# Kernel tuning notes

Hardware: AMD Instinct MI355X
Metric: run time of the kernel (lower is better)

Reference implementation:

```python
import math
import jax, jax.numpy as jnp
import numpy as np

N_NODES = 10000
N_EDGES = 160000
F_IN = 256
HID = 500
N_OUT = 100


def setup_inputs() -> dict:
    key = jax.random.key(0)
    ks = jax.random.split(key, 20)
    inp = {}
    inp['x'] = jax.random.normal(ks[0], (N_NODES, F_IN), jnp.float32)
    inp['edge_src'] = jax.random.randint(ks[1], (N_EDGES,), 0, N_NODES, jnp.int32)
    inp['edge_dst'] = jax.random.randint(ks[2], (N_EDGES,), 0, N_NODES, jnp.int32)
    inp['edge_weight'] = jax.random.uniform(ks[3], (N_EDGES,), jnp.float32)
    s1 = 1.0 / math.sqrt(F_IN)
    s2 = 1.0 / math.sqrt(HID)
    inp['W1_rel'] = jax.random.uniform(ks[4], (HID, F_IN), jnp.float32, -s1, s1)
    inp['b1'] = jax.random.uniform(ks[5], (HID,), jnp.float32, -s1, s1)
    inp['W1_root'] = jax.random.uniform(ks[6], (HID, F_IN), jnp.float32, -s1, s1)
    inp['p1_w'] = jax.random.uniform(ks[7], (HID,), jnp.float32, -s2, s2)
    inp['W2_rel'] = jax.random.uniform(ks[8], (HID, HID), jnp.float32, -s2, s2)
    inp['b2'] = jax.random.uniform(ks[9], (HID,), jnp.float32, -s2, s2)
    inp['W2_root'] = jax.random.uniform(ks[10], (HID, HID), jnp.float32, -s2, s2)
    inp['p2_w'] = jax.random.uniform(ks[11], (HID,), jnp.float32, -s2, s2)
    s3 = 1.0 / math.sqrt(1000)
    inp['lin1_W'] = jax.random.uniform(ks[12], (2000, 1000), jnp.float32, -s3, s3)
    inp['lin1_b'] = jax.random.uniform(ks[13], (2000,), jnp.float32, -s3, s3)
    s4 = 1.0 / math.sqrt(2000)
    inp['lin2_W'] = jax.random.uniform(ks[14], (4000, 2000), jnp.float32, -s4, s4)
    inp['lin2_b'] = jax.random.uniform(ks[15], (4000,), jnp.float32, -s4, s4)
    s5 = 1.0 / math.sqrt(4000)
    inp['lin3_W'] = jax.random.uniform(ks[16], (N_OUT, 4000), jnp.float32, -s5, s5)
    inp['lin3_b'] = jax.random.uniform(ks[17], (N_OUT,), jnp.float32, -s5, s5)
    return inp


def graph_conv(x, src, dst, w, W_rel, b_rel, W_root):
    # PyG GraphConv: out_i = W_rel @ sum_{j->i} w_ji * x_j + b + W_root @ x_i
    msg = x[src] * w[:, None]                              # [E, F]
    agg = jax.ops.segment_sum(msg, dst, num_segments=x.shape[0])
    return agg @ W_rel.T + b_rel + x @ W_root.T


def topk_pool(x, src, dst, w, p_w, ratio=0.5):
    # PyG TopKPooling: score = tanh(x @ p / ||p||); keep top-k; scale x by score.
    N = x.shape[0]
    k = int(math.ceil(ratio * N))
    score = jnp.tanh((x @ p_w) / jnp.linalg.norm(p_w))
    vals, perm = jax.lax.top_k(score, k)
    x_new = x[perm] * vals[:, None]
    # keep fixed-size edge list; dropped edges get weight 0 and point to node 0
    new_idx = jnp.zeros((N,), jnp.int32).at[perm].set(jnp.arange(k, dtype=jnp.int32))
    mask = jnp.zeros((N,), bool).at[perm].set(True)
    keep = mask[src] & mask[dst]
    src_new = jnp.where(keep, new_idx[src], 0)
    dst_new = jnp.where(keep, new_idx[dst], 0)
    w_new = jnp.where(keep, w, 0.0)
    return x_new, src_new, dst_new, w_new


def readout(x):
    # global max pool + global mean pool over the single graph -> [1, 2F]
    return jnp.concatenate([jnp.max(x, 0, keepdims=True), jnp.mean(x, 0, keepdims=True)], axis=1)


def reference(x, edge_src, edge_dst, edge_weight,
              W1_rel, b1, W1_root, p1_w,
              W2_rel, b2, W2_root, p2_w,
              lin1_W, lin1_b, lin2_W, lin2_b, lin3_W, lin3_b):
    h = jax.nn.relu(graph_conv(x, edge_src, edge_dst, edge_weight, W1_rel, b1, W1_root))
    h, s1, d1, w1 = topk_pool(h, edge_src, edge_dst, edge_weight, p1_w)
    x1 = readout(h)
    h = jax.nn.relu(graph_conv(h, s1, d1, w1, W2_rel, b2, W2_root))
    h, _, _, _ = topk_pool(h, s1, d1, w1, p2_w)
    x2 = readout(h)
    z = x1 + x2                                            # [1, 1000]
    z = jax.nn.relu(z @ lin1_W.T + lin1_b)
    z = jax.nn.relu(z @ lin2_W.T + lin2_b)                 # dropout is identity at eval
    return jax.nn.sigmoid(z @ lin3_W.T + lin3_b)
```

## Files before the change

kernel.cpp:

```cpp
#include <hip/hip_runtime.h>
#include <math.h>

#define NN1   10000
#define NE    160000
#define FIN   256
#define HID   500
#define K1    5000
#define NN2   5000
#define K2    2500
#define NSLAB 64
#define RORPB  79
#define RCHUNK 500

#define CSR_OFFS   0u
#define CSR_POS    10008u
#define OFF_SC1    20008u
#define OFF_SC2    30008u
#define OFF_CTR    35008u
#define ZERO_BASE  10008u
#define ZERO_LEN   25032u
#define CSR_EDGE   35040u
#define OFF_SCALE1 355040u
#define OFF_SCALE2 365040u
#define OFF_RK1    370040u
#define OFF_RK2    380040u
#define OFF_PM1    385056u
#define OFF_PS1    417056u
#define OFF_PM2    449056u
#define OFF_PS2    481056u
#define OFF_Z      513056u
#define OFF_T1     514056u
#define OFF_T2     516056u
#define OFF_INV    520056u
#define OFF_AGG    520064u
#define OFF_H      1800064u
#define OFF_XP1B   4300064u
#define OFF_XB     6175064u
#define OFF_W1RB   7455064u
#define OFF_W1TB   7519064u
#define OFF_W2RB   7583064u
#define OFF_W2TB   7708064u
#define OFF_CNT    7833088u
#define WS_FLOATS  8033120u

__device__ inline unsigned f2ord(float f) {
    unsigned u = __float_as_uint(f);
    return (u & 0x80000000u) ? ~u : (u | 0x80000000u);
}
__device__ inline unsigned long long rkey(float s, int j) {
    return ((unsigned long long)f2ord(s) << 32) | (unsigned)(0xFFFFFFFFu - (unsigned)j);
}
__device__ inline unsigned short bf16rn(float f) {
    unsigned u = __float_as_uint(f);
    u += 0x7FFFu + ((u >> 16) & 1u);
    return (unsigned short)(u >> 16);
}
__device__ inline float bf2f(unsigned short u) {
    return __uint_as_float((unsigned)u << 16);
}

typedef __attribute__((ext_vector_type(8))) short short8;
typedef __attribute__((ext_vector_type(4))) float floatx4;

__device__ inline short8 ld8g(const unsigned short* p, int gk, int K) {
    if (gk + 7 < K) return *(const short8*)p;
    unsigned short tmp[8] = {0,0,0,0,0,0,0,0};
    for (int q = 0; q < 8; ++q) if (gk + q < K) tmp[q] = p[q];
    return *(short8*)tmp;
}


__global__ __launch_bounds__(256) void k_prep(
    const float* __restrict__ x, unsigned short* __restrict__ xb,
    const float* __restrict__ w1r, unsigned short* __restrict__ w1rb,
    const float* __restrict__ w1t, unsigned short* __restrict__ w1tb,
    const float* __restrict__ w2r, unsigned short* __restrict__ w2rb,
    const float* __restrict__ w2t, unsigned short* __restrict__ w2tb,
    const float* __restrict__ p1, const float* __restrict__ p2,
    float* __restrict__ invn,
    const int* __restrict__ edst, int* __restrict__ pos) {
    __shared__ float red[256];
    int tid = threadIdx.x;
    int y = blockIdx.y;
    if (y < 5) {
        const float* s; unsigned short* d; int n4;
        switch (y) {
            case 0: s = x;   d = xb;   n4 = NN1 * FIN / 4; break;
            case 1: s = w1r; d = w1rb; n4 = HID * FIN / 4; break;
            case 2: s = w1t; d = w1tb; n4 = HID * FIN / 4; break;
            case 3: s = w2r; d = w2rb; n4 = HID * HID / 4; break;
            default: s = w2t; d = w2tb; n4 = HID * HID / 4; break;
        }
        int stride = gridDim.x * 256;
        for (int i = blockIdx.x * 256 + tid; i < n4; i += stride) {
            float4 v = *(const float4*)(s + (size_t)i * 4);
            ushort4 o;
            o.x = bf16rn(v.x); o.y = bf16rn(v.y); o.z = bf16rn(v.z); o.w = bf16rn(v.w);
            *(ushort4*)(d + (size_t)i * 4) = o;
        }
    } else if (y == 5) {
        if (blockIdx.x >= 2) return;
        const float* p = blockIdx.x ? p2 : p1;
        float s = 0.f;
        for (int i = tid; i < HID; i += 256) { float v = p[i]; s += v * v; }
        red[tid] = s; __syncthreads();
        for (int w = 128; w > 0; w >>= 1) {
            if (tid < w) red[tid] += red[tid + w];
            __syncthreads();
        }
        if (tid == 0) invn[blockIdx.x] = 1.0f / sqrtf(red[0]);
    } else {
        int stride = gridDim.x * 256;
        for (int e = blockIdx.x * 256 + tid; e < NE; e += stride)
            atomicAdd(&pos[edst[e]], 1);
    }
}

__global__ __launch_bounds__(1024) void k_scan(int* __restrict__ pos, int* __restrict__ offs) {
    __shared__ int tot[1024];
    int t = threadIdx.x;
    int base = t * 10;
    int loc[10]; int s = 0;
    #pragma unroll
    for (int q = 0; q < 10; ++q) {
        int v = (base + q < NN1) ? pos[base + q] : 0;
        loc[q] = s; s += v;
    }
    tot[t] = s; __syncthreads();
    for (int d = 1; d < 1024; d <<= 1) {
        int v = (t >= d) ? tot[t - d] : 0;
        __syncthreads();
        tot[t] += v;
        __syncthreads();
    }
    int excl = (t == 0) ? 0 : tot[t - 1];
    #pragma unroll
    for (int q = 0; q < 10; ++q)
        if (base + q < NN1) { int o = excl + loc[q]; offs[base + q] = o; pos[base + q] = o; }
    if (t == 1023) offs[NN1] = tot[1023];
}

__global__ __launch_bounds__(256) void k_fill(
    const int* __restrict__ src, const int* __restrict__ dst,
    const float* __restrict__ w, int* __restrict__ pos,
    int2* __restrict__ ce) {
    int e = blockIdx.x * 256 + threadIdx.x;
    if (e >= NE) return;
    int slot = atomicAdd(&pos[dst[e]], 1);
    ce[slot] = make_int2(src[e], __float_as_int(w[e]));
}

__global__ __launch_bounds__(256) void k_gather1(
    const unsigned short* __restrict__ xb, const int* __restrict__ offs,
    const int2* __restrict__ ce, unsigned short* __restrict__ aggb) {
    int wave = (blockIdx.x * 256 + threadIdx.x) >> 6;
    int lane = threadIdx.x & 63;
    if (wave >= NN1) return;
    int b = offs[wave], e = offs[wave + 1];
    float4 a0 = make_float4(0.f, 0.f, 0.f, 0.f);
    float4 a1 = make_float4(0.f, 0.f, 0.f, 0.f);
    int p = b;
    for (; p + 1 < e; p += 2) {
        int2 e0 = ce[p], e1 = ce[p + 1];
        float w0 = __int_as_float(e0.y), w1 = __int_as_float(e1.y);
        ushort4 u0 = *(const ushort4*)(xb + (size_t)e0.x * FIN + lane * 4);
        ushort4 u1 = *(const ushort4*)(xb + (size_t)e1.x * FIN + lane * 4);
        a0.x += bf2f(u0.x) * w0; a0.y += bf2f(u0.y) * w0;
        a0.z += bf2f(u0.z) * w0; a0.w += bf2f(u0.w) * w0;
        a1.x += bf2f(u1.x) * w1; a1.y += bf2f(u1.y) * w1;
        a1.z += bf2f(u1.z) * w1; a1.w += bf2f(u1.w) * w1;
    }
    if (p < e) {
        int2 e0 = ce[p];
        float w0 = __int_as_float(e0.y);
        ushort4 u0 = *(const ushort4*)(xb + (size_t)e0.x * FIN + lane * 4);
        a0.x += bf2f(u0.x) * w0; a0.y += bf2f(u0.y) * w0;
        a0.z += bf2f(u0.z) * w0; a0.w += bf2f(u0.w) * w0;
    }
    ushort4 o;
    o.x = bf16rn(a0.x + a1.x); o.y = bf16rn(a0.y + a1.y);
    o.z = bf16rn(a0.z + a1.z); o.w = bf16rn(a0.w + a1.w);
    *(ushort4*)(aggb + (size_t)wave * FIN + lane * 4) = o;
}

#define GBK 64
__global__ __launch_bounds__(256) void k_gemm_bf16(
    const unsigned short* __restrict__ A1, const unsigned short* __restrict__ B1,
    const unsigned short* __restrict__ A2, const unsigned short* __restrict__ B2,
    const float* __restrict__ bias, const float* __restrict__ pv,
    unsigned short* __restrict__ C, float* __restrict__ score,
    int M, int N, int Ka, int Kb, int nbyRow) {
    __shared__ unsigned short As[2][64 * 64];
    __shared__ unsigned short Bs[2][64 * 64];
    int tid = threadIdx.x;
    int b = blockIdx.x;
    int xcd = b & 7, seq = b >> 3;
    int colT = seq & 7;
    int rowT = xcd + 8 * (seq >> 3);
    if (rowT >= nbyRow) return;
    int row0 = rowT * 64, col0 = colT * 64;
    int lane = tid & 63, wid = tid >> 6;
    int waveM = wid & 1, waveN = wid >> 1;
    int quad = lane >> 4, mrow = lane & 15;
    int m7 = mrow & 7;
    floatx4 acc[2][2] = {};

    int sr = tid >> 2;
    int ca = (tid & 3) * 2;
    int s7 = sr & 7;
    int c0 = (ca ^ s7) * 8;
    int c1 = ((ca + 1) ^ s7) * 8;
    int sbase = sr * 64;

    int nka = (Ka + GBK - 1) / GBK;
    int nkb = (Kb + GBK - 1) / GBK;
    int niter = nka + nkb;

    short8 z8 = {0,0,0,0,0,0,0,0};
    short8 paA = z8, paB = z8, pbA = z8, pbB = z8;

    auto fetch = [&](int t) {
        int ph = (t >= nka);
        const unsigned short* A = ph ? A2 : A1;
        const unsigned short* B = ph ? B2 : B1;
        int K = ph ? Kb : Ka;
        int gk = (ph ? t - nka : t) * GBK + ca * 8;
        int gr = row0 + sr, gn = col0 + sr;
        paA = z8; paB = z8; pbA = z8; pbB = z8;
        if (gr < M) {
            const unsigned short* p = A + (size_t)gr * K + gk;
            paA = ld8g(p, gk, K); paB = ld8g(p + 8, gk + 8, K);
        }
        if (gn < N) {
            const unsigned short* p = B + (size_t)gn * K + gk;
            pbA = ld8g(p, gk, K); pbB = ld8g(p + 8, gk + 8, K);
        }
    };
    auto commit = [&](int buf) {
        *(short8*)&As[buf][sbase + c0] = paA;
        *(short8*)&As[buf][sbase + c1] = paB;
        *(short8*)&Bs[buf][sbase + c0] = pbA;
        *(short8*)&Bs[buf][sbase + c1] = pbB;
    };

    fetch(0);
    commit(0);
    if (niter > 1) fetch(1);
    __syncthreads();

    for (int it = 0; it < niter; ++it) {
        int cur = it & 1;
        if (it + 1 < niter) commit(cur ^ 1);
        if (it + 2 < niter) fetch(it + 2);
        #pragma unroll
        for (int half = 0; half < 2; ++half) {
            int qc = half * 4 + quad;
            int qoff = (qc ^ m7) * 8;
            short8 bfr[2];
            #pragma unroll
            for (int nt = 0; nt < 2; ++nt)
                bfr[nt] = *(short8*)&Bs[cur][(waveN * 32 + nt * 16 + mrow) * 64 + qoff];
            #pragma unroll
            for (int mt = 0; mt < 2; ++mt) {
                short8 afr = *(short8*)&As[cur][(waveM * 32 + mt * 16 + mrow) * 64 + qoff];
                #pragma unroll
                for (int nt = 0; nt < 2; ++nt)
                    acc[mt][nt] = __builtin_amdgcn_mfma_f32_16x16x32_bf16(
                        afr, bfr[nt], acc[mt][nt], 0, 0, 0);
            }
        }
        __syncthreads();
    }
    float ps[2][4] = {};
    #pragma unroll
    for (int nt = 0; nt < 2; ++nt) {
        int col = col0 + waveN * 32 + nt * 16 + mrow;
        if (col >= N) continue;
        float bv = bias[col];
        float pc = pv[col];
        #pragma unroll
        for (int mt = 0; mt < 2; ++mt) {
            int rbase = row0 + waveM * 32 + mt * 16 + quad * 4;
            #pragma unroll
            for (int r = 0; r < 4; ++r) {
                float v = fmaxf(acc[mt][nt][r] + bv, 0.f);
                int row = rbase + r;
                if (row < M) C[(size_t)row * N + col] = bf16rn(v);
                ps[mt][r] += v * pc;
            }
        }
    }
    #pragma unroll
    for (int mt = 0; mt < 2; ++mt)
        #pragma unroll
        for (int r = 0; r < 4; ++r) {
            float v = ps[mt][r];
            v += __shfl_xor(v, 1, 64); v += __shfl_xor(v, 2, 64);
            v += __shfl_xor(v, 4, 64); v += __shfl_xor(v, 8, 64);
            if (mrow == 0) {
                int row = row0 + waveM * 32 + mt * 16 + quad * 4 + r;
                if (row < M) atomicAdd(&score[row], v);
            }
        }
}

__global__ __launch_bounds__(256) void k_rank_partial(
    const float* __restrict__ score, int* __restrict__ cntp, int Nn) {
    __shared__ unsigned long long kj[RCHUNK];
    int j0 = blockIdx.y * RCHUNK;
    int jn = min(Nn - j0, RCHUNK);
    for (int t = threadIdx.x; t < jn; t += 256)
        kj[t] = rkey(score[j0 + t], j0 + t);
    __syncthreads();
    int i = blockIdx.x * 256 + threadIdx.x;
    if (i >= Nn) return;
    unsigned long long ki = rkey(score[i], i);
    int c = 0;
    #pragma unroll 4
    for (int q = 0; q < jn; ++q)
        c += (kj[q] > ki) ? 1 : 0;
    cntp[(size_t)blockIdx.y * Nn + i] = c;
}

__global__ __launch_bounds__(256) void k_gather_pool(
    const unsigned short* __restrict__ Hb, const float* __restrict__ score,
    const float* __restrict__ invn,
    const int* __restrict__ cntp, int Nn, int nchunk, int kk,
    int* __restrict__ rank_out, unsigned short* __restrict__ Xb) {
    int wave = (blockIdx.x * 256 + threadIdx.x) >> 6;
    int lane = threadIdx.x & 63;
    int nw = gridDim.x * 4;
    for (int i = wave; i < Nn; i += nw) {
        int c = (lane < nchunk) ? cntp[(size_t)lane * Nn + i] : 0;
        for (int off = 32; off > 0; off >>= 1) c += __shfl_down(c, off, 64);
        c = __shfl(c, 0, 64);
        int r = (c < kk) ? c : -1;
        if (lane == 0) rank_out[i] = r;
        if (r < 0) continue;
        float sc = tanhf(score[i] * invn[0]);
        const ushort4* src = (const ushort4*)(Hb + (size_t)i * HID);
        ushort4* dst = (ushort4*)(Xb + (size_t)r * HID);
        ushort4 u = src[lane];
        ushort4 o;
        o.x = bf16rn(bf2f(u.x) * sc); o.y = bf16rn(bf2f(u.y) * sc);
        o.z = bf16rn(bf2f(u.z) * sc); o.w = bf16rn(bf2f(u.w) * sc);
        dst[lane] = o;
        if (lane < HID / 4 - 64) {
            ushort4 u2 = src[lane + 64];
            ushort4 o2;
            o2.x = bf16rn(bf2f(u2.x) * sc); o2.y = bf16rn(bf2f(u2.y) * sc);
            o2.z = bf16rn(bf2f(u2.z) * sc); o2.w = bf16rn(bf2f(u2.w) * sc);
            dst[lane + 64] = o2;
        }
    }
}

__global__ __launch_bounds__(256) void k_rank_fin2(
    const float* __restrict__ score, const float* __restrict__ invn,
    const int* __restrict__ cntp, int Nn, int nchunk, int kk,
    int* __restrict__ rank_out, float* __restrict__ scale_out) {
    int i = blockIdx.x * 256 + threadIdx.x;
    if (i >= Nn) return;
    int t = 0;
    for (int q = 0; q < nchunk; ++q) t += cntp[(size_t)q * Nn + i];
    rank_out[i] = (t < kk) ? t : -1;
    scale_out[i] = tanhf(score[i] * invn[0]);
}

__device__ void readout_slab(const unsigned short* __restrict__ X, int rows, int rpb,
                             int slabY, int colHalf,
                             float* __restrict__ pmax, float* __restrict__ psum) {
    __shared__ float4 lmx[4][64];
    __shared__ float4 lsm[4][64];
    int lane = threadIdx.x & 63;
    int rgrp = threadIdx.x >> 6;
    int c4 = colHalf * 64 + lane;
    int r0 = slabY * rpb;
    int r1 = min(rows, r0 + rpb);
    float4 mx = make_float4(-INFINITY, -INFINITY, -INFINITY, -INFINITY);
    float4 sm = make_float4(0.f, 0.f, 0.f, 0.f);
    if (c4 < HID / 4) {
        for (int r = r0 + rgrp; r < r1; r += 4) {
            ushort4 u = *(const ushort4*)(X + (size_t)r * HID + c4 * 4);
            float vx = bf2f(u.x), vy = bf2f(u.y), vz = bf2f(u.z), vw = bf2f(u.w);
            mx.x = fmaxf(mx.x, vx); mx.y = fmaxf(mx.y, vy);
            mx.z = fmaxf(mx.z, vz); mx.w = fmaxf(mx.w, vw);
            sm.x += vx; sm.y += vy; sm.z += vz; sm.w += vw;
        }
    }
    lmx[rgrp][lane] = mx; lsm[rgrp][lane] = sm;
    __syncthreads();
    if (rgrp == 0 && c4 < HID / 4) {
        #pragma unroll
        for (int g = 1; g < 4; ++g) {
            float4 m2 = lmx[g][lane], s2 = lsm[g][lane];
            mx.x = fmaxf(mx.x, m2.x); mx.y = fmaxf(mx.y, m2.y);
            mx.z = fmaxf(mx.z, m2.z); mx.w = fmaxf(mx.w, m2.w);
            sm.x += s2.x; sm.y += s2.y; sm.z += s2.z; sm.w += s2.w;
        }
        *(float4*)(pmax + (size_t)slabY * HID + c4 * 4) = mx;
        *(float4*)(psum + (size_t)slabY * HID + c4 * 4) = sm;
    }
}

__global__ __launch_bounds__(256) void k_g2r1(
    const unsigned short* __restrict__ xp1, const int* __restrict__ offs,
    const int2* __restrict__ ce, const int* __restrict__ rank,
    unsigned short* __restrict__ aggb,
    float* __restrict__ pm1, float* __restrict__ ps1) {
    if (blockIdx.x < 2500) {
        int wave = (blockIdx.x * 256 + threadIdx.x) >> 6;
        int lane = threadIdx.x & 63;
        int rd = rank[wave];
        if (rd < 0) return;
        int b = offs[wave], e = offs[wave + 1];
        int c1 = 256 + lane * 4;
        float a0 = 0.f, a1 = 0.f, a2 = 0.f, a3 = 0.f;
        float b0 = 0.f, b1v = 0.f, b2 = 0.f, b3 = 0.f;
        int2 nxt = (b < e) ? ce[b] : make_int2(0, 0);
        for (int p = b; p < e; ++p) {
            int2 cur = nxt;
            if (p + 1 < e) nxt = ce[p + 1];
            int rs = rank[cur.x];
            if (rs < 0) continue;
            float we = __int_as_float(cur.y);
            const unsigned short* row = xp1 + (size_t)rs * HID;
            ushort4 u = *(const ushort4*)(row + lane * 4);
            a0 += bf2f(u.x) * we; a1 += bf2f(u.y) * we;
            a2 += bf2f(u.z) * we; a3 += bf2f(u.w) * we;
            if (c1 < HID) {
                ushort4 u2 = *(const ushort4*)(row + c1);
                b0 += bf2f(u2.x) * we; b1v += bf2f(u2.y) * we;
                b2 += bf2f(u2.z) * we; b3 += bf2f(u2.w) * we;
            }
        }
        unsigned short* o = aggb + (size_t)rd * HID;
        ushort4 o1; o1.x = bf16rn(a0); o1.y = bf16rn(a1); o1.z = bf16rn(a2); o1.w = bf16rn(a3);
        *(ushort4*)(o + lane * 4) = o1;
        if (c1 < HID) {
            ushort4 o2; o2.x = bf16rn(b0); o2.y = bf16rn(b1v); o2.z = bf16rn(b2); o2.w = bf16rn(b3);
            *(ushort4*)(o + c1) = o2;
        }
    } else {
        int b = blockIdx.x - 2500;
        readout_slab(xp1, K1, RORPB, b >> 1, b & 1, pm1, ps1);
    }
}

__global__ __launch_bounds__(256) void k_readout2(
    const unsigned short* __restrict__ hb, const int* __restrict__ rank2,
    const float* __restrict__ scale2,
    float* __restrict__ pm2, float* __restrict__ ps2,
    const float* __restrict__ pm1, const float* __restrict__ ps1,
    float* __restrict__ z, int* __restrict__ donectr) {
    __shared__ float4 lmx[4][64];
    __shared__ float4 lsm[4][64];
    __shared__ int flag;
    int tid = threadIdx.x;
    int lane = tid & 63;
    int rgrp = tid >> 6;
    int slabY = blockIdx.x >> 1, colHalf = blockIdx.x & 1;
    int c4 = colHalf * 64 + lane;
    int r0 = slabY * RORPB;
    int r1 = min(NN2, r0 + RORPB);
    float4 mx = make_float4(-INFINITY, -INFINITY, -INFINITY, -INFINITY);
    float4 sm = make_float4(0.f, 0.f, 0.f, 0.f);
    if (c4 < HID / 4) {
        for (int r = r0 + rgrp; r < r1; r += 4) {
            if (rank2[r] < 0) continue;
            float sc = scale2[r];
            ushort4 u = *(const ushort4*)(hb + (size_t)r * HID + c4 * 4);
            float vx = bf2f(u.x) * sc, vy = bf2f(u.y) * sc;
            float vz = bf2f(u.z) * sc, vw = bf2f(u.w) * sc;
            mx.x = fmaxf(mx.x, vx); mx.y = fmaxf(mx.y, vy);
            mx.z = fmaxf(mx.z, vz); mx.w = fmaxf(mx.w, vw);
            sm.x += vx; sm.y += vy; sm.z += vz; sm.w += vw;
        }
    }
    lmx[rgrp][lane] = mx; lsm[rgrp][lane] = sm;
    __syncthreads();
    if (rgrp == 0 && c4 < HID / 4) {
        #pragma unroll
        for (int g = 1; g < 4; ++g) {
            float4 m2 = lmx[g][lane], s2 = lsm[g][lane];
            mx.x = fmaxf(mx.x, m2.x); mx.y = fmaxf(mx.y, m2.y);
            mx.z = fmaxf(mx.z, m2.z); mx.w = fmaxf(mx.w, m2.w);
            sm.x += s2.x; sm.y += s2.y; sm.z += s2.z; sm.w += s2.w;
        }
        *(float4*)(pm2 + (size_t)slabY * HID + c4 * 4) = mx;
        *(float4*)(ps2 + (size_t)slabY * HID + c4 * 4) = sm;
    }
    if (tid == 0) {
        __threadfence();
        flag = (atomicAdd(donectr, 1) == (int)gridDim.x - 1) ? 1 : 0;
    }
    __syncthreads();
    if (!flag) return;
    __threadfence();
    for (int j = tid; j < HID; j += 256) {
        float m1 = -INFINITY, s1 = 0.f, m2v = -INFINITY, s2v = 0.f;
        for (int s = 0; s < NSLAB; ++s) {
            m1 = fmaxf(m1, pm1[(size_t)s * HID + j]); s1 += ps1[(size_t)s * HID + j];
            m2v = fmaxf(m2v, pm2[(size_t)s * HID + j]); s2v += ps2[(size_t)s * HID + j];
        }
        z[j] = m1 + m2v;
        z[HID + j] = s1 * (1.0f / (float)K1) + s2v * (1.0f / (float)K2);
    }
}

__global__ __launch_bounds__(256) void k_mv(
    const float* __restrict__ v, const float* __restrict__ W,
    const float* __restrict__ bias, float* __restrict__ y,
    int rowsN, int K, int act) {
    int wave = (blockIdx.x * 256 + threadIdx.x) >> 6;
    int lane = threadIdx.x & 63;
    if (wave >= rowsN) return;
    const float* wr = W + (size_t)wave * K;
    float s = 0.f;
    for (int c = lane * 4; c < K; c += 256) {
        float4 a = *(const float4*)(wr + c);
        float4 xv = *(const float4*)(v + c);
        s += a.x * xv.x + a.y * xv.y + a.z * xv.z + a.w * xv.w;
    }
    for (int off = 32; off > 0; off >>= 1) s += __shfl_down(s, off, 64);
    if (lane == 0) {
        float r = s + bias[wave];
        y[wave] = (act == 0) ? fmaxf(r, 0.f) : 1.f / (1.f + expf(-r));
    }
}

extern "C" void kernel_launch(void* const* d_in, const int* in_sizes, int n_in,
                              void* d_out, int out_size, void* d_ws, size_t ws_size,
                              hipStream_t stream) {
    const float* x      = (const float*)d_in[0];
    const int*   esrc   = (const int*)d_in[1];
    const int*   edst   = (const int*)d_in[2];
    const float* ew     = (const float*)d_in[3];
    const float* W1_rel = (const float*)d_in[4];
    const float* b1     = (const float*)d_in[5];
    const float* W1_root= (const float*)d_in[6];
    const float* p1     = (const float*)d_in[7];
    const float* W2_rel = (const float*)d_in[8];
    const float* b2     = (const float*)d_in[9];
    const float* W2_root= (const float*)d_in[10];
    const float* p2     = (const float*)d_in[11];
    const float* l1W    = (const float*)d_in[12];
    const float* l1b    = (const float*)d_in[13];
    const float* l2W    = (const float*)d_in[14];
    const float* l2b    = (const float*)d_in[15];
    const float* l3W    = (const float*)d_in[16];
    const float* l3b    = (const float*)d_in[17];
    float* out = (float*)d_out;
    float* ws  = (float*)d_ws;

    if (ws_size < (size_t)WS_FLOATS * sizeof(float)) return;

    int*            offs   = (int*)(ws + CSR_OFFS);
    int*            pos    = (int*)(ws + CSR_POS);
    float*          score1 = ws + OFF_SC1;
    float*          score2 = ws + OFF_SC2;
    int*            ctr    = (int*)(ws + OFF_CTR);
    int2*           ce     = (int2*)(ws + CSR_EDGE);
    float*          scale2 = ws + OFF_SCALE2;
    int*            rk1    = (int*)(ws + OFF_RK1);
    int*            rk2    = (int*)(ws + OFF_RK2);
    float*          pm1    = ws + OFF_PM1;
    float*          ps1    = ws + OFF_PS1;
    float*          pm2    = ws + OFF_PM2;
    float*          ps2    = ws + OFF_PS2;
    float*          zbuf   = ws + OFF_Z;
    float*          t1     = ws + OFF_T1;
    float*          t2     = ws + OFF_T2;
    float*          invn   = ws + OFF_INV;
    int*            cntp   = (int*)(ws + OFF_CNT);
    unsigned short* aggb   = (unsigned short*)(ws + OFF_AGG);
    unsigned short* hb     = (unsigned short*)(ws + OFF_H);
    unsigned short* xp1b   = (unsigned short*)(ws + OFF_XP1B);
    unsigned short* xb     = (unsigned short*)(ws + OFF_XB);
    unsigned short* w1rb   = (unsigned short*)(ws + OFF_W1RB);
    unsigned short* w1tb   = (unsigned short*)(ws + OFF_W1TB);
    unsigned short* w2rb   = (unsigned short*)(ws + OFF_W2RB);
    unsigned short* w2tb   = (unsigned short*)(ws + OFF_W2TB);

    hipMemsetAsync(ws + ZERO_BASE, 0, (size_t)ZERO_LEN * sizeof(float), stream);

    k_prep<<<dim3(640, 7), 256, 0, stream>>>(
        x, xb, W1_rel, w1rb, W1_root, w1tb, W2_rel, w2rb, W2_root, w2tb,
        p1, p2, invn, edst, pos);
    k_scan<<<1, 1024, 0, stream>>>(pos, offs);
    k_fill<<<(NE + 255) / 256, 256, 0, stream>>>(esrc, edst, ew, pos, ce);

    k_gather1<<<(NN1 * 64) / 256, 256, 0, stream>>>(xb, offs, ce, aggb);
    {
        int nby = (NN1 + 63) / 64;
        int nblk = 64 * ((nby + 7) / 8);
        k_gemm_bf16<<<nblk, 256, 0, stream>>>(
            aggb, w1rb, xb, w1tb, b1, p1, hb, score1, NN1, HID, FIN, FIN, nby);
    }

    k_rank_partial<<<dim3((NN1 + 255) / 256, NN1 / RCHUNK), 256, 0, stream>>>(
        score1, cntp, NN1);
    k_gather_pool<<<1250, 256, 0, stream>>>(
        hb, score1, invn + 0, cntp, NN1, NN1 / RCHUNK, K1, rk1, xp1b);

    k_g2r1<<<2500 + 2 * NSLAB, 256, 0, stream>>>(xp1b, offs, ce, rk1, aggb, pm1, ps1);
    {
        int nby = (NN2 + 63) / 64;
        int nblk = 64 * ((nby + 7) / 8);
        k_gemm_bf16<<<nblk, 256, 0, stream>>>(
            aggb, w2rb, xp1b, w2tb, b2, p2, hb, score2, NN2, HID, HID, HID, nby);
    }

    k_rank_partial<<<dim3((NN2 + 255) / 256, NN2 / RCHUNK), 256, 0, stream>>>(
        score2, cntp, NN2);
    k_rank_fin2<<<(NN2 + 255) / 256, 256, 0, stream>>>(
        score2, invn + 1, cntp, NN2, NN2 / RCHUNK, K2, rk2, scale2);

    k_readout2<<<2 * NSLAB, 256, 0, stream>>>(
        hb, rk2, scale2, pm2, ps2, pm1, ps1, zbuf, ctr + 3);

    k_mv<<<(2000 * 64) / 256, 256, 0, stream>>>(zbuf, l1W, l1b, t1, 2000, 1000, 0);
    k_mv<<<(4000 * 64) / 256, 256, 0, stream>>>(t1, l2W, l2b, t2, 4000, 2000, 0);
    k_mv<<<(100 * 64) / 256, 256, 0, stream>>>(t2, l3W, l3b, out, 100, 4000, 1);
}
```

Before: 315.9 us.

## Fuse second top-k ranking and scale into readout kernel

Removes the separate partial-rank and rank-finalize launches for the second pooling stage. Each readout block now ranks its own slab of rows by comparing score keys against all 5000 scores staged in shared memory, and computes the tanh scale locally. This saves two kernel launches and the round trip of the count buffer through global memory. In exchange, every block redoes the ranking comparisons for its rows (about 79x5000 per block) and uses about 20 KB of shared memory.

```diff
diff --git a/kernel.cpp b/kernel.cpp
--- a/kernel.cpp
+++ b/kernel.cpp
@@ -20,10 +20,7 @@
 #define ZERO_BASE  10008u
 #define ZERO_LEN   25032u
 #define CSR_EDGE   35040u
-#define OFF_SCALE1 355040u
-#define OFF_SCALE2 365040u
-#define OFF_RK1    370040u
-#define OFF_RK2    380040u
+#define OFF_RK1X   370040u
 #define OFF_PM1    385056u
 #define OFF_PS1    417056u
 #define OFF_PM2    449056u
@@ -353,18 +350,6 @@
             dst[lane + 64] = o2;
         }
     }
-}
-
-__global__ __launch_bounds__(256) void k_rank_fin2(
-    const float* __restrict__ score, const float* __restrict__ invn,
-    const int* __restrict__ cntp, int Nn, int nchunk, int kk,
-    int* __restrict__ rank_out, float* __restrict__ scale_out) {
-    int i = blockIdx.x * 256 + threadIdx.x;
-    if (i >= Nn) return;
-    int t = 0;
-    for (int q = 0; q < nchunk; ++q) t += cntp[(size_t)q * Nn + i];
-    rank_out[i] = (t < kk) ? t : -1;
-    scale_out[i] = tanhf(score[i] * invn[0]);
 }
 
 __device__ void readout_slab(const unsigned short* __restrict__ X, int rows, int rpb,
@@ -447,28 +432,55 @@
     }
 }
 
-__global__ __launch_bounds__(256) void k_readout2(
-    const unsigned short* __restrict__ hb, const int* __restrict__ rank2,
-    const float* __restrict__ scale2,
+__global__ __launch_bounds__(256) void k_ro2f(
+    const unsigned short* __restrict__ hb, const float* __restrict__ score,
+    const float* __restrict__ invn,
     float* __restrict__ pm2, float* __restrict__ ps2,
     const float* __restrict__ pm1, const float* __restrict__ ps1,
     float* __restrict__ z, int* __restrict__ donectr) {
+    __shared__ unsigned long long kj[2500];
+    __shared__ int rk_s[RORPB];
+    __shared__ float sc_s[RORPB];
     __shared__ float4 lmx[4][64];
     __shared__ float4 lsm[4][64];
     __shared__ int flag;
     int tid = threadIdx.x;
+    int slabY = blockIdx.x >> 1, colHalf = blockIdx.x & 1;
+    int r0 = slabY * RORPB;
+    int rl = tid >> 1, half = tid & 1;
+    int row = r0 + rl;
+    bool act = (rl < RORPB) && (row < NN2);
+    unsigned long long ki = act ? rkey(score[row], row) : 0ULL;
+    int cnt = 0;
+    for (int c = 0; c < 2; ++c) {
+        int j0 = c * 2500;
+        __syncthreads();
+        for (int j = tid; j < 2500; j += 256)
+            kj[j] = rkey(score[j0 + j], j0 + j);
+        __syncthreads();
+        if (act) {
+            int bb = half * 1250;
+            #pragma unroll 4
+            for (int q = 0; q < 1250; ++q)
+                cnt += (kj[bb + q] > ki) ? 1 : 0;
+        }
+    }
+    int tot = cnt + __shfl_xor(cnt, 1, 64);
+    if (act && half == 0) {
+        rk_s[rl] = (tot < K2) ? 1 : 0;
+        sc_s[rl] = tanhf(score[row] * invn[0]);
+    }
+    __syncthreads();
     int lane = tid & 63;
     int rgrp = tid >> 6;
-    int slabY = blockIdx.x >> 1, colHalf = blockIdx.x & 1;
     int c4 = colHalf * 64 + lane;
-    int r0 = slabY * RORPB;
     int r1 = min(NN2, r0 + RORPB);
     float4 mx = make_float4(-INFINITY, -INFINITY, -INFINITY, -INFINITY);
     float4 sm = make_float4(0.f, 0.f, 0.f, 0.f);
     if (c4 < HID / 4) {
         for (int r = r0 + rgrp; r < r1; r += 4) {
-            if (rank2[r] < 0) continue;
-            float sc = scale2[r];
+            if (!rk_s[r - r0]) continue;
+            float sc = sc_s[r - r0];
             ushort4 u = *(const ushort4*)(hb + (size_t)r * HID + c4 * 4);
             float vx = bf2f(u.x) * sc, vy = bf2f(u.y) * sc;
             float vz = bf2f(u.z) * sc, vw = bf2f(u.w) * sc;
@@ -561,9 +573,7 @@
     float*          score2 = ws + OFF_SC2;
     int*            ctr    = (int*)(ws + OFF_CTR);
     int2*           ce     = (int2*)(ws + CSR_EDGE);
-    float*          scale2 = ws + OFF_SCALE2;
-    int*            rk1    = (int*)(ws + OFF_RK1);
-    int*            rk2    = (int*)(ws + OFF_RK2);
+    int*            rk1    = (int*)(ws + OFF_RK1X);
     float*          pm1    = ws + OFF_PM1;
     float*          ps1    = ws + OFF_PS1;
     float*          pm2    = ws + OFF_PM2;
@@ -611,13 +621,8 @@
             aggb, w2rb, xp1b, w2tb, b2, p2, hb, score2, NN2, HID, HID, HID, nby);
     }
 
-    k_rank_partial<<<dim3((NN2 + 255) / 256, NN2 / RCHUNK), 256, 0, stream>>>(
-        score2, cntp, NN2);
-    k_rank_fin2<<<(NN2 + 255) / 256, 256, 0, stream>>>(
-        score2, invn + 1, cntp, NN2, NN2 / RCHUNK, K2, rk2, scale2);
-
-    k_readout2<<<2 * NSLAB, 256, 0, stream>>>(
-        hb, rk2, scale2, pm2, ps2, pm1, ps1, zbuf, ctr + 3);
+    k_ro2f<<<2 * NSLAB, 256, 0, stream>>>(
+        hb, score2, invn + 1, pm2, ps2, pm1, ps1, zbuf, ctr + 3);
 
     k_mv<<<(2000 * 64) / 256, 256, 0, stream>>>(zbuf, l1W, l1b, t1, 2000, 1000, 0);
     k_mv<<<(4000 * 64) / 256, 256, 0, stream>>>(t1, l2W, l2b, t2, 4000, 2000, 0);
```

Measured after the change: 366.5 us. 16.0% more time.

## Fuse top-k rank counting with pool gather into one kernel

Applied to the files above, without the earlier changes.

Replaces the two-pass rank computation (per-chunk partial counts written to a global buffer, then a reduce-and-gather kernel) with a single kernel. In it, each wave counts for four nodes across all keys staged in shared memory, reduces with shuffles, then writes the rank, scale and gathered row. This removes a kernel launch per pooling stage and the partial-count buffer traffic. In exchange, each block re-stages every score key into LDS, so total rank work moves from many small blocks to fewer, longer blocks with O(N) shared reads each.

```diff
diff --git a/kernel.cpp b/kernel.cpp
--- a/kernel.cpp
+++ b/kernel.cpp
@@ -10,7 +10,7 @@
 #define K2    2500
 #define NSLAB 64
 #define RORPB  79
-#define RCHUNK 500
+#define PRCH  2500
 
 #define CSR_OFFS   0u
 #define CSR_POS    10008u
@@ -20,7 +20,6 @@
 #define ZERO_BASE  10008u
 #define ZERO_LEN   25032u
 #define CSR_EDGE   35040u
-#define OFF_SCALE1 355040u
 #define OFF_SCALE2 365040u
 #define OFF_RK1    370040u
 #define OFF_RK2    380040u
@@ -40,7 +39,6 @@
 #define OFF_W1TB   7519064u
 #define OFF_W2RB   7583064u
 #define OFF_W2TB   7708064u
-#define OFF_CNT    7833088u
 #define WS_FLOATS  8033120u
 
 __device__ inline unsigned f2ord(float f) {
@@ -304,42 +302,53 @@
         }
 }
 
-__global__ __launch_bounds__(256) void k_rank_partial(
-    const float* __restrict__ score, int* __restrict__ cntp, int Nn) {
-    __shared__ unsigned long long kj[RCHUNK];
-    int j0 = blockIdx.y * RCHUNK;
-    int jn = min(Nn - j0, RCHUNK);
-    for (int t = threadIdx.x; t < jn; t += 256)
-        kj[t] = rkey(score[j0 + t], j0 + t);
-    __syncthreads();
-    int i = blockIdx.x * 256 + threadIdx.x;
-    if (i >= Nn) return;
-    unsigned long long ki = rkey(score[i], i);
-    int c = 0;
-    #pragma unroll 4
-    for (int q = 0; q < jn; ++q)
-        c += (kj[q] > ki) ? 1 : 0;
-    cntp[(size_t)blockIdx.y * Nn + i] = c;
-}
-
-__global__ __launch_bounds__(256) void k_gather_pool(
+__global__ __launch_bounds__(256) void k_poolrank(
     const unsigned short* __restrict__ Hb, const float* __restrict__ score,
-    const float* __restrict__ invn,
-    const int* __restrict__ cntp, int Nn, int nchunk, int kk,
-    int* __restrict__ rank_out, unsigned short* __restrict__ Xb) {
-    int wave = (blockIdx.x * 256 + threadIdx.x) >> 6;
-    int lane = threadIdx.x & 63;
-    int nw = gridDim.x * 4;
-    for (int i = wave; i < Nn; i += nw) {
-        int c = (lane < nchunk) ? cntp[(size_t)lane * Nn + i] : 0;
+    const float* __restrict__ invn, int Nn, int kk,
+    int* __restrict__ rank_out, float* __restrict__ scale_out,
+    unsigned short* __restrict__ Xb) {
+    __shared__ unsigned long long kj[PRCH];
+    int tid = threadIdx.x;
+    int lane = tid & 63;
+    int w = blockIdx.x * 4 + (tid >> 6);
+    int i0 = w * 4;
+    unsigned long long ki[4];
+    #pragma unroll
+    for (int r = 0; r < 4; ++r) {
+        int i = i0 + r;
+        ki[r] = (i < Nn) ? rkey(score[i], i) : 0xFFFFFFFFFFFFFFFFull;
+    }
+    int cnt[4] = {0, 0, 0, 0};
+    int nch = (Nn + PRCH - 1) / PRCH;
+    for (int c = 0; c < nch; ++c) {
+        int j0 = c * PRCH;
+        int jn = min(Nn - j0, PRCH);
+        __syncthreads();
+        for (int j = tid; j < jn; j += 256)
+            kj[j] = rkey(score[j0 + j], j0 + j);
+        __syncthreads();
+        for (int j = lane; j < jn; j += 64) {
+            unsigned long long kv = kj[j];
+            #pragma unroll
+            for (int r = 0; r < 4; ++r) cnt[r] += (kv > ki[r]) ? 1 : 0;
+        }
+    }
+    #pragma unroll
+    for (int r = 0; r < 4; ++r) {
+        int c = cnt[r];
         for (int off = 32; off > 0; off >>= 1) c += __shfl_down(c, off, 64);
-        c = __shfl(c, 0, 64);
-        int r = (c < kk) ? c : -1;
-        if (lane == 0) rank_out[i] = r;
-        if (r < 0) continue;
+        cnt[r] = __shfl(c, 0, 64);
+    }
+    for (int r = 0; r < 4; ++r) {
+        int i = i0 + r;
+        if (i >= Nn) break;
+        int rk = (cnt[r] < kk) ? cnt[r] : -1;
+        if (lane == 0) rank_out[i] = rk;
+        if (scale_out && lane == 1) scale_out[i] = tanhf(score[i] * invn[0]);
+        if (!Xb || rk < 0) continue;
         float sc = tanhf(score[i] * invn[0]);
         const ushort4* src = (const ushort4*)(Hb + (size_t)i * HID);
-        ushort4* dst = (ushort4*)(Xb + (size_t)r * HID);
+        ushort4* dst = (ushort4*)(Xb + (size_t)rk * HID);
         ushort4 u = src[lane];
         ushort4 o;
         o.x = bf16rn(bf2f(u.x) * sc); o.y = bf16rn(bf2f(u.y) * sc);
@@ -353,18 +362,6 @@
             dst[lane + 64] = o2;
         }
     }
-}
-
-__global__ __launch_bounds__(256) void k_rank_fin2(
-    const float* __restrict__ score, const float* __restrict__ invn,
-    const int* __restrict__ cntp, int Nn, int nchunk, int kk,
-    int* __restrict__ rank_out, float* __restrict__ scale_out) {
-    int i = blockIdx.x * 256 + threadIdx.x;
-    if (i >= Nn) return;
-    int t = 0;
-    for (int q = 0; q < nchunk; ++q) t += cntp[(size_t)q * Nn + i];
-    rank_out[i] = (t < kk) ? t : -1;
-    scale_out[i] = tanhf(score[i] * invn[0]);
 }
 
 __device__ void readout_slab(const unsigned short* __restrict__ X, int rows, int rpb,
@@ -572,7 +569,6 @@
     float*          t1     = ws + OFF_T1;
     float*          t2     = ws + OFF_T2;
     float*          invn   = ws + OFF_INV;
-    int*            cntp   = (int*)(ws + OFF_CNT);
     unsigned short* aggb   = (unsigned short*)(ws + OFF_AGG);
     unsigned short* hb     = (unsigned short*)(ws + OFF_H);
     unsigned short* xp1b   = (unsigned short*)(ws + OFF_XP1B);
@@ -598,10 +594,8 @@
             aggb, w1rb, xb, w1tb, b1, p1, hb, score1, NN1, HID, FIN, FIN, nby);
     }
 
-    k_rank_partial<<<dim3((NN1 + 255) / 256, NN1 / RCHUNK), 256, 0, stream>>>(
-        score1, cntp, NN1);
-    k_gather_pool<<<1250, 256, 0, stream>>>(
-        hb, score1, invn + 0, cntp, NN1, NN1 / RCHUNK, K1, rk1, xp1b);
+    k_poolrank<<<625, 256, 0, stream>>>(
+        hb, score1, invn + 0, NN1, K1, rk1, (float*)nullptr, xp1b);
 
     k_g2r1<<<2500 + 2 * NSLAB, 256, 0, stream>>>(xp1b, offs, ce, rk1, aggb, pm1, ps1);
     {
@@ -611,10 +605,8 @@
             aggb, w2rb, xp1b, w2tb, b2, p2, hb, score2, NN2, HID, HID, HID, nby);
     }
 
-    k_rank_partial<<<dim3((NN2 + 255) / 256, NN2 / RCHUNK), 256, 0, stream>>>(
-        score2, cntp, NN2);
-    k_rank_fin2<<<(NN2 + 255) / 256, 256, 0, stream>>>(
-        score2, invn + 1, cntp, NN2, NN2 / RCHUNK, K2, rk2, scale2);
+    k_poolrank<<<313, 256, 0, stream>>>(
+        hb, score2, invn + 1, NN2, K2, rk2, scale2, (unsigned short*)nullptr);
 
     k_readout2<<<2 * NSLAB, 256, 0, stream>>>(
         hb, rk2, scale2, pm2, ps2, pm1, ps1, zbuf, ctr + 3);
```

Result: slower. 323.6 us (+2.4%).
